# Optimization experiments

Measured on AMD Instinct MI355X. Metric: run time of the kernel, lower is better.

## Reference

```python
import jax, jax.numpy as jnp
import numpy as np

H = 16
D_MODEL = 1024
D_K = D_MODEL // H
B, S = 4, 2048


def setup_inputs() -> dict:
    key = jax.random.key(0)
    ks = jax.random.split(key, 12)
    scale = 1.0 / np.sqrt(D_MODEL)
    inp = {
        "query": jax.random.normal(ks[0], (B, S, D_MODEL), jnp.float32),
        "key_in": jax.random.normal(ks[1], (B, S, D_MODEL), jnp.float32),
        "value": jax.random.normal(ks[2], (B, S, D_MODEL), jnp.float32),
        "mask": jax.random.randint(ks[3], (B, 1, S, S), 0, 2, jnp.int32),
    }
    # 4 Linear(d_model, d_model) layers: Wq, Wk, Wv, Wo (+ biases)
    names = ["q", "k", "v", "o"]
    for i, n in enumerate(names):
        inp[f"W{n}"] = jax.random.normal(ks[4 + i], (D_MODEL, D_MODEL), jnp.float32) * scale
        inp[f"b{n}"] = jax.random.normal(ks[8 + i], (D_MODEL,), jnp.float32) * scale
    return inp


def reference(query, key_in, value, mask, Wq, bq, Wk, bk, Wv, bv, Wo, bo):
    # Linear projections then split heads: [B,S,D] -> [B,H,S,Dk]
    def proj(x, W, b):
        y = jnp.einsum("bsd,ed->bse", x, W) + b  # torch Linear: x @ W.T + b
        return y.reshape(B, S, H, D_K).transpose(0, 2, 1, 3)

    q = proj(query, Wq, bq)
    k = proj(key_in, Wk, bk)
    v = proj(value, Wv, bv)

    scores = jnp.einsum("bhqd,bhkd->bhqk", q, k) / jnp.sqrt(jnp.float32(D_K))
    scores = jnp.where(mask == 0, jnp.float32(-1e9), scores)
    p_attn = jax.nn.softmax(scores, axis=-1)
    # dropout is identity in eval mode
    x = jnp.einsum("bhqk,bhkd->bhqd", p_attn, v)
    x = x.transpose(0, 2, 1, 3).reshape(B, S, D_MODEL)
    return jnp.einsum("bsd,ed->bse", x, Wo) + bo
```

## Files before the change

kernel.cpp:

```cpp
#include <hip/hip_runtime.h>
#include <hip/hip_bf16.h>

typedef __bf16 bf16_t;
typedef __attribute__((ext_vector_type(8))) __bf16 bf16x8;
typedef __attribute__((ext_vector_type(4))) __bf16 bf16x4;
typedef __attribute__((ext_vector_type(4))) float f32x4;

#define GAS __attribute__((address_space(1)))
#define LAS __attribute__((address_space(3)))

__device__ __forceinline__ void async_copy16(const bf16_t* g, bf16_t* l) {
    __builtin_amdgcn_global_load_lds((const GAS void*)g, (LAS void*)l, 16, 0, 0);
}

__global__ __launch_bounds__(256) void convert_kernel(
    const float* __restrict__ src, bf16_t* __restrict__ dst, int n)
{
    int i = (blockIdx.x * 256 + threadIdx.x) * 8;
    if (i >= n) return;
    f32x4 f0 = *(const f32x4*)(src + i);
    f32x4 f1 = *(const f32x4*)(src + i + 4);
    bf16x8 v;
#pragma unroll
    for (int j = 0; j < 4; j++) { v[j] = (bf16_t)f0[j]; v[4 + j] = (bf16_t)f1[j]; }
    *(bf16x8*)&dst[i] = v;
}

__global__ __launch_bounds__(256) void pack_mask_kernel(
    const int* __restrict__ mask, unsigned long long* __restrict__ out)
{
    int i = blockIdx.x * 256 + threadIdx.x;
    unsigned long long bits = __ballot(mask[i] != 0);
    if ((threadIdx.x & 63) == 0) out[i >> 6] = bits;
}

template<int MODE>
__global__ __launch_bounds__(256, 2) void gemm_nt(
    const bf16_t* __restrict__ A, const bf16_t* __restrict__ W,
    const float* __restrict__ bias, void* __restrict__ out_, float oscale)
{
    __shared__ __align__(16) bf16_t Als[128 * 32];
    __shared__ __align__(16) bf16_t Bls[128 * 32];

    const int tid  = threadIdx.x;
    const int wave = tid >> 6, lane = tid & 63;
    const int quad = lane >> 4, lq = lane & 15;
    const int wm = wave >> 1, wn = wave & 1;
    const int tm = blockIdx.x * 128, tn = blockIdx.y * 128;
    const int K = 1024;

    const bf16_t* gA0 = A + (size_t)(tm + wave * 32 + (lane >> 2)) * K + (lane & 3) * 8;
    const bf16_t* gA1 = gA0 + (size_t)16 * K;
    const bf16_t* gB0 = W + (size_t)(tn + wave * 32 + (lane >> 2)) * K + (lane & 3) * 8;
    const bf16_t* gB1 = gB0 + (size_t)16 * K;
    bf16_t* lA0 = &Als[(wave * 32) * 32];
    bf16_t* lA1 = &Als[(wave * 32 + 16) * 32];
    bf16_t* lB0 = &Bls[(wave * 32) * 32];
    bf16_t* lB1 = &Bls[(wave * 32 + 16) * 32];

    f32x4 acc[4][4] = {};

    for (int k0 = 0; k0 < K; k0 += 32) {
        __syncthreads();
        async_copy16(gA0, lA0);
        async_copy16(gA1, lA1);
        async_copy16(gB0, lB0);
        async_copy16(gB1, lB1);
        gA0 += 32; gA1 += 32; gB0 += 32; gB1 += 32;
        __syncthreads();

        bf16x8 af[4], bfr[4];
#pragma unroll
        for (int i = 0; i < 4; i++) {
            af[i]  = *(const bf16x8*)&Als[(wm * 64 + i * 16 + lq) * 32 + quad * 8];
            bfr[i] = *(const bf16x8*)&Bls[(wn * 64 + i * 16 + lq) * 32 + quad * 8];
        }
#pragma unroll
        for (int i = 0; i < 4; i++)
#pragma unroll
            for (int j = 0; j < 4; j++) {
                if (MODE == 2)
                    acc[i][j] = __builtin_amdgcn_mfma_f32_16x16x32_bf16(bfr[j], af[i], acc[i][j], 0, 0, 0);
                else
                    acc[i][j] = __builtin_amdgcn_mfma_f32_16x16x32_bf16(af[i], bfr[j], acc[i][j], 0, 0, 0);
            }
    }

    float* outf = (float*)out_;
    bf16_t* outb = (bf16_t*)out_;
#pragma unroll
    for (int i = 0; i < 4; i++)
#pragma unroll
        for (int j = 0; j < 4; j++)
#pragma unroll
            for (int r = 0; r < 4; r++) {
                float v = acc[i][j][r];
                if (MODE == 0) {
                    int row = tm + wm * 64 + i * 16 + quad * 4 + r;
                    int col = tn + wn * 64 + j * 16 + lq;
                    outf[(size_t)row * 1024 + col] = (v + bias[col]) * oscale;
                } else if (MODE == 1) {
                    int row = tm + wm * 64 + i * 16 + quad * 4 + r;
                    int col = tn + wn * 64 + j * 16 + lq;
                    v = (v + bias[col]) * oscale;
                    int b = row >> 11, s = row & 2047;
                    int h = col >> 6,  dk = col & 63;
                    outb[(((size_t)(b * 16 + h) * 2048 + s) << 6) + dk] = (bf16_t)v;
                } else {
                    int n = tn + wn * 64 + j * 16 + quad * 4 + r;
                    int m = tm + wm * 64 + i * 16 + lq;
                    v = (v + bias[n]) * oscale;
                    int b = m >> 11, s = m & 2047;
                    int h = n >> 6,  dk = n & 63;
                    outb[((size_t)((b * 16 + h) * 64 + dk) << 11) + s] = (bf16_t)v;
                }
            }
}

#define LDK 72
#define LDV 72
#define LDP 72

__global__ __launch_bounds__(256, 4) void attn_kernel(
    const bf16_t* __restrict__ Q, const bf16_t* __restrict__ Kh,
    const bf16_t* __restrict__ Vt, const unsigned int* __restrict__ mp,
    bf16_t* __restrict__ X)
{
    __shared__ __align__(16) bf16_t Kls[64 * LDK];
    __shared__ __align__(16) bf16_t Vls[64 * LDV];
    __shared__ __align__(16) bf16_t Pls[4][32 * LDP];

    const int tid  = threadIdx.x;
    const int wave = tid >> 6, lane = tid & 63;
    const int quad = lane >> 4, lq = lane & 15;
    const int bh = blockIdx.y;
    const int b  = bh >> 4, h = bh & 15;
    const int qwv = blockIdx.x * 128 + wave * 32;

    bf16x8 qf[2][2];
#pragma unroll
    for (int qs = 0; qs < 2; qs++) {
        const bf16_t* qptr = Q + ((size_t)bh * 2048 + qwv + qs * 16 + lq) * 64 + quad * 8;
        qf[qs][0] = *(const bf16x8*)qptr;
        qf[qs][1] = *(const bf16x8*)(qptr + 32);
    }

    f32x4 o[2][4] = {};
    f32x4 ls[2] = {};

    const int sr = tid >> 3, sc = tid & 7;
    const bf16_t* gK0 = Kh + ((size_t)bh * 2048 + sr) * 64 + sc * 8;
    const bf16_t* gK1 = gK0 + 32 * 64;
    const bf16_t* gV0 = Vt + ((size_t)bh * 64 + sr) * 2048 + sc * 8;
    const bf16_t* gV1 = gV0 + 32 * 2048;
    bf16_t* lK0 = &Kls[sr * LDK + sc * 8];
    bf16_t* lK1 = &Kls[(sr + 32) * LDK + sc * 8];
    bf16_t* lV0 = &Vls[sr * LDV + sc * 8];
    bf16_t* lV1 = &Vls[(sr + 32) * LDV + sc * 8];

    const unsigned int* mr0 = mp + ((size_t)(b << 11) + qwv + lq) * 64;

    bf16x8 ks0 = *(const bf16x8*)gK0, ks1 = *(const bf16x8*)gK1;
    bf16x8 vs0 = *(const bf16x8*)gV0, vs1 = *(const bf16x8*)gV1;

    for (int kt = 0; kt < 32; kt++) {
        __syncthreads();
        *(bf16x8*)lK0 = ks0; *(bf16x8*)lK1 = ks1;
        *(bf16x8*)lV0 = vs0; *(bf16x8*)lV1 = vs1;
        __syncthreads();
        if (kt < 31) {
            gK0 += 4096; gK1 += 4096; gV0 += 64; gV1 += 64;
            ks0 = *(const bf16x8*)gK0; ks1 = *(const bf16x8*)gK1;
            vs0 = *(const bf16x8*)gV0; vs1 = *(const bf16x8*)gV1;
        }
        unsigned int w[2][2];
        w[0][0] = mr0[2 * kt];        w[0][1] = mr0[2 * kt + 1];
        w[1][0] = mr0[2 * kt + 1024]; w[1][1] = mr0[2 * kt + 1025];

        bf16_t* pb = &Pls[wave][0];
#pragma unroll
        for (int nt = 0; nt < 4; nt++) {
            const bf16_t* krow = &Kls[(nt * 16 + lq) * LDK];
            bf16x8 kf0 = *(const bf16x8*)(krow + quad * 8);
            bf16x8 kf1 = *(const bf16x8*)(krow + 32 + quad * 8);
#pragma unroll
            for (int qs = 0; qs < 2; qs++) {
                f32x4 z = {};
                z = __builtin_amdgcn_mfma_f32_16x16x32_bf16(kf0, qf[qs][0], z, 0, 0, 0);
                z = __builtin_amdgcn_mfma_f32_16x16x32_bf16(kf1, qf[qs][1], z, 0, 0, 0);
                unsigned int wq = w[qs][nt >> 1] >> ((nt & 1) * 16 + quad * 4);
                bf16x4 pk;
#pragma unroll
                for (int r = 0; r < 4; r++) {
                    float sv = ((wq >> r) & 1) ? z[r] : -1e9f;
                    float p = __expf(sv);
                    ls[qs][r] += p;
                    pk[r] = (bf16_t)p;
                }
                *(bf16x4*)&pb[(qs * 16 + lq) * LDP + nt * 16 + quad * 4] = pk;
            }
        }

#pragma unroll
        for (int c = 0; c < 2; c++) {
            bf16x8 pf0 = *(const bf16x8*)&pb[lq * LDP + c * 32 + quad * 8];
            bf16x8 pf1 = *(const bf16x8*)&pb[(16 + lq) * LDP + c * 32 + quad * 8];
#pragma unroll
            for (int dt = 0; dt < 4; dt++) {
                bf16x8 vf = *(const bf16x8*)&Vls[(dt * 16 + lq) * LDV + c * 32 + quad * 8];
                o[0][dt] = __builtin_amdgcn_mfma_f32_16x16x32_bf16(pf0, vf, o[0][dt], 0, 0, 0);
                o[1][dt] = __builtin_amdgcn_mfma_f32_16x16x32_bf16(pf1, vf, o[1][dt], 0, 0, 0);
            }
        }
    }

#pragma unroll
    for (int qs = 0; qs < 2; qs++) {
        float l = (ls[qs][0] + ls[qs][1]) + (ls[qs][2] + ls[qs][3]);
        l += __shfl_xor(l, 16);
        l += __shfl_xor(l, 32);
        float rl[4];
#pragma unroll
        for (int r = 0; r < 4; r++) {
            float lv = __shfl(l, quad * 4 + r);
            rl[r] = (lv > 0.f) ? 1.0f / lv : 0.f;
        }
#pragma unroll
        for (int dt = 0; dt < 4; dt++)
#pragma unroll
            for (int r = 0; r < 4; r++) {
                int qrow = qwv + qs * 16 + quad * 4 + r;
                X[((size_t)(b * 2048) + qrow) * 1024 + h * 64 + dt * 16 + lq] =
                    (bf16_t)(o[qs][dt][r] * rl[r]);
            }
    }
}

extern "C" void kernel_launch(void* const* d_in, const int* in_sizes, int n_in,
                              void* d_out, int out_size, void* d_ws, size_t ws_size,
                              hipStream_t stream)
{
    const float* query  = (const float*)d_in[0];
    const float* key_in = (const float*)d_in[1];
    const float* value  = (const float*)d_in[2];
    const int*   mask   = (const int*)d_in[3];

    char* ws = (char*)d_ws;
    const size_t SZ  = (size_t)8192 * 1024 * 2;
    const size_t MPK = (size_t)2 * 1024 * 1024;
    const size_t WSZ = (size_t)1024 * 1024 * 2;
    bf16_t* C   = (bf16_t*)(ws);
    bf16_t* Qb  = (bf16_t*)(ws + SZ);
    bf16_t* Kb  = (bf16_t*)(ws + 2 * SZ);
    bf16_t* Vtb = (bf16_t*)(ws + 3 * SZ);
    unsigned long long* mpack = (unsigned long long*)(ws + 4 * SZ);
    bf16_t* Wc[4];
    for (int i = 0; i < 4; i++)
        Wc[i] = (bf16_t*)(ws + 4 * SZ + MPK + i * WSZ);

    const size_t NEED = 4 * SZ + MPK + 4 * WSZ;
    if (ws_size < NEED) return;

    const int NACT = 8192 * 1024;
    for (int i = 0; i < 4; i++)
        convert_kernel<<<512, 256, 0, stream>>>((const float*)d_in[4 + 2 * i],
                                                Wc[i], 1024 * 1024);
    pack_mask_kernel<<<65536, 256, 0, stream>>>(mask, mpack);

    dim3 gg(64, 8);
    convert_kernel<<<4096, 256, 0, stream>>>(query, C, NACT);
    gemm_nt<1><<<gg, 256, 0, stream>>>(C, Wc[0], (const float*)d_in[5], Qb, 0.125f);
    convert_kernel<<<4096, 256, 0, stream>>>(key_in, C, NACT);
    gemm_nt<1><<<gg, 256, 0, stream>>>(C, Wc[1], (const float*)d_in[7], Kb, 1.0f);
    convert_kernel<<<4096, 256, 0, stream>>>(value, C, NACT);
    gemm_nt<2><<<gg, 256, 0, stream>>>(C, Wc[2], (const float*)d_in[9], Vtb, 1.0f);

    attn_kernel<<<dim3(16, 64), 256, 0, stream>>>(Qb, Kb, Vtb,
                                                  (const unsigned int*)mpack, C);
    gemm_nt<0><<<gg, 256, 0, stream>>>(C, Wc[3], (const float*)d_in[11], d_out, 1.0f);
}
```

Before: 443.0 us.

## Rewrite attention with 32x32 MFMA, 64 queries per wave, swizzled LDS

Switches the attention kernel from 16x16x32 to 32x32x16 bf16 MFMA tiles and gives each wave 64 query rows instead of 32. Each block now covers 256 queries, so there are half as many blocks and each staged K/V tile is reused across more queries, cutting global and LDS traffic per query. It also XOR-swizzles the K/V LDS columns, changes the P row stride, and reads the packed mask as 64-bit words. The costs are higher register pressure (launch bounds drop to 2 blocks per unit), more LDS for the P buffer, and only 512 blocks to spread across the GPU.

```diff
diff --git a/kernel.cpp b/kernel.cpp
--- a/kernel.cpp
+++ b/kernel.cpp
@@ -5,6 +5,7 @@
 typedef __attribute__((ext_vector_type(8))) __bf16 bf16x8;
 typedef __attribute__((ext_vector_type(4))) __bf16 bf16x4;
 typedef __attribute__((ext_vector_type(4))) float f32x4;
+typedef __attribute__((ext_vector_type(16))) float f32x16;
 
 #define GAS __attribute__((address_space(1)))
 #define LAS __attribute__((address_space(3)))
@@ -119,49 +120,56 @@
 
 #define LDK 72
 #define LDV 72
-#define LDP 72
-
-__global__ __launch_bounds__(256, 4) void attn_kernel(
+#define LDP 68
+
+__global__ __launch_bounds__(256, 2) void attn_kernel(
     const bf16_t* __restrict__ Q, const bf16_t* __restrict__ Kh,
     const bf16_t* __restrict__ Vt, const unsigned int* __restrict__ mp,
     bf16_t* __restrict__ X)
 {
     __shared__ __align__(16) bf16_t Kls[64 * LDK];
     __shared__ __align__(16) bf16_t Vls[64 * LDV];
-    __shared__ __align__(16) bf16_t Pls[4][32 * LDP];
+    __shared__ __align__(16) bf16_t Pls[4][64 * LDP];
 
     const int tid  = threadIdx.x;
     const int wave = tid >> 6, lane = tid & 63;
-    const int quad = lane >> 4, lq = lane & 15;
+    const int l31  = lane & 31;
+    const int hi8  = (lane >> 5) * 8, hi4 = (lane >> 5) * 4;
+    const int xr8  = lane & 8;
     const int bh = blockIdx.y;
     const int b  = bh >> 4, h = bh & 15;
-    const int qwv = blockIdx.x * 128 + wave * 32;
-
-    bf16x8 qf[2][2];
-#pragma unroll
-    for (int qs = 0; qs < 2; qs++) {
-        const bf16_t* qptr = Q + ((size_t)bh * 2048 + qwv + qs * 16 + lq) * 64 + quad * 8;
-        qf[qs][0] = *(const bf16x8*)qptr;
-        qf[qs][1] = *(const bf16x8*)(qptr + 32);
-    }
-
-    f32x4 o[2][4] = {};
-    f32x4 ls[2] = {};
+    const int qb = blockIdx.x * 256 + wave * 64;
+
+    bf16x8 qf[2][4];
+#pragma unroll
+    for (int qg = 0; qg < 2; qg++) {
+        const bf16_t* qp = Q + ((size_t)bh * 2048 + qb + qg * 32 + l31) * 64 + hi8;
+#pragma unroll
+        for (int c = 0; c < 4; c++) qf[qg][c] = *(const bf16x8*)(qp + c * 16);
+    }
+
+    f32x16 od[2][2] = {};
+    float lsum[2] = {0.f, 0.f};
 
     const int sr = tid >> 3, sc = tid & 7;
     const bf16_t* gK0 = Kh + ((size_t)bh * 2048 + sr) * 64 + sc * 8;
     const bf16_t* gK1 = gK0 + 32 * 64;
     const bf16_t* gV0 = Vt + ((size_t)bh * 64 + sr) * 2048 + sc * 8;
     const bf16_t* gV1 = gV0 + 32 * 2048;
-    bf16_t* lK0 = &Kls[sr * LDK + sc * 8];
-    bf16_t* lK1 = &Kls[(sr + 32) * LDK + sc * 8];
-    bf16_t* lV0 = &Vls[sr * LDV + sc * 8];
-    bf16_t* lV1 = &Vls[(sr + 32) * LDV + sc * 8];
-
-    const unsigned int* mr0 = mp + ((size_t)(b << 11) + qwv + lq) * 64;
+    const int swc = (sc * 8) ^ (sr & 8);
+    bf16_t* lK0 = &Kls[sr * LDK + swc];
+    bf16_t* lK1 = &Kls[(sr + 32) * LDK + swc];
+    bf16_t* lV0 = &Vls[sr * LDV + swc];
+    bf16_t* lV1 = &Vls[(sr + 32) * LDV + swc];
+
+    const unsigned long long* mq0 =
+        (const unsigned long long*)mp + ((size_t)(b << 11) + qb + l31) * 32;
+    const unsigned long long* mq1 = mq0 + 32 * 32;
 
     bf16x8 ks0 = *(const bf16x8*)gK0, ks1 = *(const bf16x8*)gK1;
     bf16x8 vs0 = *(const bf16x8*)gV0, vs1 = *(const bf16x8*)gV1;
+
+    bf16_t* pw = &Pls[wave][0];
 
     for (int kt = 0; kt < 32; kt++) {
         __syncthreads();
@@ -173,65 +181,74 @@
             ks0 = *(const bf16x8*)gK0; ks1 = *(const bf16x8*)gK1;
             vs0 = *(const bf16x8*)gV0; vs1 = *(const bf16x8*)gV1;
         }
-        unsigned int w[2][2];
-        w[0][0] = mr0[2 * kt];        w[0][1] = mr0[2 * kt + 1];
-        w[1][0] = mr0[2 * kt + 1024]; w[1][1] = mr0[2 * kt + 1025];
-
-        bf16_t* pb = &Pls[wave][0];
-#pragma unroll
-        for (int nt = 0; nt < 4; nt++) {
-            const bf16_t* krow = &Kls[(nt * 16 + lq) * LDK];
-            bf16x8 kf0 = *(const bf16x8*)(krow + quad * 8);
-            bf16x8 kf1 = *(const bf16x8*)(krow + 32 + quad * 8);
-#pragma unroll
-            for (int qs = 0; qs < 2; qs++) {
-                f32x4 z = {};
-                z = __builtin_amdgcn_mfma_f32_16x16x32_bf16(kf0, qf[qs][0], z, 0, 0, 0);
-                z = __builtin_amdgcn_mfma_f32_16x16x32_bf16(kf1, qf[qs][1], z, 0, 0, 0);
-                unsigned int wq = w[qs][nt >> 1] >> ((nt & 1) * 16 + quad * 4);
-                bf16x4 pk;
-#pragma unroll
-                for (int r = 0; r < 4; r++) {
-                    float sv = ((wq >> r) & 1) ? z[r] : -1e9f;
-                    float p = __expf(sv);
-                    ls[qs][r] += p;
-                    pk[r] = (bf16_t)p;
+        unsigned long long mw[2] = { mq0[kt], mq1[kt] };
+
+#pragma unroll
+        for (int kh = 0; kh < 2; kh++) {
+            bf16x8 kf[4];
+            const bf16_t* krow = &Kls[(kh * 32 + l31) * LDK];
+#pragma unroll
+            for (int c = 0; c < 4; c++)
+                kf[c] = *(const bf16x8*)(krow + ((c * 16 + hi8) ^ xr8));
+
+#pragma unroll
+            for (int qg = 0; qg < 2; qg++) {
+                f32x16 z = {};
+                z = __builtin_amdgcn_mfma_f32_32x32x16_bf16(kf[0], qf[qg][0], z, 0, 0, 0);
+                z = __builtin_amdgcn_mfma_f32_32x32x16_bf16(kf[1], qf[qg][1], z, 0, 0, 0);
+                z = __builtin_amdgcn_mfma_f32_32x32x16_bf16(kf[2], qf[qg][2], z, 0, 0, 0);
+                z = __builtin_amdgcn_mfma_f32_32x32x16_bf16(kf[3], qf[qg][3], z, 0, 0, 0);
+                unsigned int mbits = (unsigned int)(mw[qg] >> (kh * 32 + hi4));
+                float ls = 0.f;
+#pragma unroll
+                for (int p = 0; p < 4; p++) {
+                    bf16x4 pk;
+#pragma unroll
+                    for (int r = 0; r < 4; r++) {
+                        float sv = ((mbits >> (8 * p + r)) & 1) ? z[4 * p + r] : -1e9f;
+                        float e = __expf(sv);
+                        ls += e;
+                        pk[r] = (bf16_t)e;
+                    }
+                    *(bf16x4*)&pw[(qg * 32 + l31) * LDP + kh * 32 + 8 * p + hi4] = pk;
                 }
-                *(bf16x4*)&pb[(qs * 16 + lq) * LDP + nt * 16 + quad * 4] = pk;
-            }
+                lsum[qg] += ls;
+            }
+
+            bf16x8 pf[2][2];
+#pragma unroll
+            for (int qg = 0; qg < 2; qg++) {
+                const bf16_t* prow = &pw[(qg * 32 + l31) * LDP + kh * 32 + hi8];
+                pf[qg][0] = *(const bf16x8*)(prow);
+                pf[qg][1] = *(const bf16x8*)(prow + 16);
+            }
+#pragma unroll
+            for (int c = 0; c < 2; c++)
+#pragma unroll
+                for (int dt = 0; dt < 2; dt++) {
+                    bf16x8 vf = *(const bf16x8*)&Vls[(dt * 32 + l31) * LDV +
+                                                     ((kh * 32 + c * 16 + hi8) ^ xr8)];
+                    od[0][dt] = __builtin_amdgcn_mfma_f32_32x32x16_bf16(vf, pf[0][c], od[0][dt], 0, 0, 0);
+                    od[1][dt] = __builtin_amdgcn_mfma_f32_32x32x16_bf16(vf, pf[1][c], od[1][dt], 0, 0, 0);
+                }
         }
-
-#pragma unroll
-        for (int c = 0; c < 2; c++) {
-            bf16x8 pf0 = *(const bf16x8*)&pb[lq * LDP + c * 32 + quad * 8];
-            bf16x8 pf1 = *(const bf16x8*)&pb[(16 + lq) * LDP + c * 32 + quad * 8];
-#pragma unroll
-            for (int dt = 0; dt < 4; dt++) {
-                bf16x8 vf = *(const bf16x8*)&Vls[(dt * 16 + lq) * LDV + c * 32 + quad * 8];
-                o[0][dt] = __builtin_amdgcn_mfma_f32_16x16x32_bf16(pf0, vf, o[0][dt], 0, 0, 0);
-                o[1][dt] = __builtin_amdgcn_mfma_f32_16x16x32_bf16(pf1, vf, o[1][dt], 0, 0, 0);
-            }
-        }
-    }
-
-#pragma unroll
-    for (int qs = 0; qs < 2; qs++) {
-        float l = (ls[qs][0] + ls[qs][1]) + (ls[qs][2] + ls[qs][3]);
-        l += __shfl_xor(l, 16);
-        l += __shfl_xor(l, 32);
-        float rl[4];
-#pragma unroll
-        for (int r = 0; r < 4; r++) {
-            float lv = __shfl(l, quad * 4 + r);
-            rl[r] = (lv > 0.f) ? 1.0f / lv : 0.f;
-        }
-#pragma unroll
-        for (int dt = 0; dt < 4; dt++)
-#pragma unroll
-            for (int r = 0; r < 4; r++) {
-                int qrow = qwv + qs * 16 + quad * 4 + r;
-                X[((size_t)(b * 2048) + qrow) * 1024 + h * 64 + dt * 16 + lq] =
-                    (bf16_t)(o[qs][dt][r] * rl[r]);
+    }
+
+#pragma unroll
+    for (int qg = 0; qg < 2; qg++) {
+        float l = lsum[qg] + __shfl_xor(lsum[qg], 32);
+        float rl = (l > 0.f) ? 1.0f / l : 0.f;
+        int qrow = qb + qg * 32 + l31;
+        bf16_t* xp = X + ((size_t)(b * 2048) + qrow) * 1024 + h * 64 + hi4;
+#pragma unroll
+        for (int dt = 0; dt < 2; dt++)
+#pragma unroll
+            for (int p = 0; p < 4; p++) {
+                bf16x4 ov;
+#pragma unroll
+                for (int r = 0; r < 4; r++)
+                    ov[r] = (bf16_t)(od[qg][dt][p * 4 + r] * rl);
+                *(bf16x4*)(xp + dt * 32 + p * 8) = ov;
             }
     }
 }
@@ -275,7 +292,7 @@
     convert_kernel<<<4096, 256, 0, stream>>>(value, C, NACT);
     gemm_nt<2><<<gg, 256, 0, stream>>>(C, Wc[2], (const float*)d_in[9], Vtb, 1.0f);
 
-    attn_kernel<<<dim3(16, 64), 256, 0, stream>>>(Qb, Kb, Vtb,
-                                                  (const unsigned int*)mpack, C);
+    attn_kernel<<<dim3(8, 64), 256, 0, stream>>>(Qb, Kb, Vtb,
+                                                 (const unsigned int*)mpack, C);
     gemm_nt<0><<<gg, 256, 0, stream>>>(C, Wc[3], (const float*)d_in[11], d_out, 1.0f);
 }
```

Result: slower. 469.4 us (+6.0%).
